# Kernel tuning notes

Hardware: AMD Instinct MI355X
Metric: run time of the kernel (lower is better)

## Reference

```python
import jax, jax.numpy as jnp
import numpy as np

B, N, D = 2, 4096, 256
H = 8
HD = D // H  # head dim = 32
DFF = 4 * D


def _layer_norm(x):
    # Matches source: (x - mean) / (std + 1e-6), std is population std (ddof=0)
    m = jnp.mean(x, axis=-1, keepdims=True)
    s = jnp.std(x, axis=-1, keepdims=True)
    return (x - m) / (s + 1e-6)


def setup_inputs() -> dict:
    key = jax.random.key(0)
    ks = jax.random.split(key, 11)
    sd = 1.0 / np.sqrt(D)
    sf = 1.0 / np.sqrt(DFF)
    return {
        "embeddings_in": jax.random.normal(ks[0], (B, N, D), dtype=jnp.float32),
        "Wq": jax.random.normal(ks[1], (D, D), dtype=jnp.float32) * sd,
        "bq": jnp.zeros((D,), dtype=jnp.float32),
        "Wk": jax.random.normal(ks[2], (D, D), dtype=jnp.float32) * sd,
        "bk": jnp.zeros((D,), dtype=jnp.float32),
        "Wv": jax.random.normal(ks[3], (D, D), dtype=jnp.float32) * sd,
        "bv": jnp.zeros((D,), dtype=jnp.float32),
        "Wo": jax.random.normal(ks[4], (D, D), dtype=jnp.float32) * sd,
        "bo": jnp.zeros((D,), dtype=jnp.float32),
        "W1": jax.random.normal(ks[5], (D, DFF), dtype=jnp.float32) * sd,
        "b1": jnp.zeros((DFF,), dtype=jnp.float32),
        "W2": jax.random.normal(ks[6], (DFF, D), dtype=jnp.float32) * sf,
        "b2": jnp.zeros((D,), dtype=jnp.float32),
    }


def reference(embeddings_in, Wq, bq, Wk, bk, Wv, bv, Wo, bo, W1, b1, W2, b2):
    x = embeddings_in
    xn1 = _layer_norm(x)
    # QKV projections, split into heads: [B,N,D] -> [B,H,N,HD]
    def heads(t):
        return jnp.transpose(t.reshape(B, N, H, HD), (0, 2, 1, 3))
    q = heads(xn1 @ Wq + bq)
    k = heads(xn1 @ Wk + bk)
    v = heads(xn1 @ Wv + bv)
    scores = jnp.einsum('bhnd,bhmd->bhnm', q, k) / jnp.sqrt(jnp.float32(HD))
    attn = jax.nn.softmax(scores, axis=-1)
    heads_out = jnp.einsum('bhnm,bhmd->bhnd', attn, v)
    attn_out = jnp.transpose(heads_out, (0, 2, 1, 3)).reshape(B, N, D)
    attn_out = attn_out @ Wo + bo  # dropout is identity in eval
    x_skip = attn_out + x
    xn2 = _layer_norm(x_skip)
    mlp = jax.nn.gelu(xn2 @ W1 + b1) @ W2 + b2
    return mlp + x_skip
```

## Files before the change

kernel.cpp:

```cpp
#include <hip/hip_runtime.h>
#include <hip/hip_bf16.h>

#define Bb 2
#define Nn 4096
#define Dd 256
#define Hh 8
#define HDh 32
#define DFFd 1024
#define MT (Bb*Nn)
#define Tt ((size_t)MT * Dd)
#define SPLIT 4
#define KVB (Nn / SPLIT)
#define NSTP (KVB / 64)

typedef __attribute__((ext_vector_type(8))) short short8;
typedef __attribute__((ext_vector_type(4))) float f32x4;
typedef __attribute__((address_space(1))) const unsigned int gu32;
typedef __attribute__((address_space(3))) unsigned int lu32;

__device__ __forceinline__ void gll16(const ushort* g, ushort* l) {
  __builtin_amdgcn_global_load_lds((gu32*)g, (lu32*)l, 16, 0, 0);
}
__device__ __forceinline__ float bf2f(ushort u){
  union { unsigned int i; float f; } v; v.i = ((unsigned int)u) << 16; return v.f;
}
__device__ __forceinline__ ushort f2bf(float f){
  union { float f; unsigned int i; } v; v.f = f;
  unsigned int r = v.i + 0x7fffu + ((v.i >> 16) & 1u);
  return (ushort)(r >> 16);
}
__device__ __forceinline__ int ars(int r){ return r * 64 + (r >> 3) * 32; }

__global__ __launch_bounds__(256) void prep_kernel(
    const float* __restrict__ Wq, const float* __restrict__ Wk,
    const float* __restrict__ Wv, const float* __restrict__ Wo,
    const float* __restrict__ W1, const float* __restrict__ W2,
    const float* __restrict__ bq, const float* __restrict__ bk,
    const float* __restrict__ bv, ushort* __restrict__ wt,
    float* __restrict__ bqkv)
{
  const int bid = blockIdx.x, t = threadIdx.x;
  if (bid == 192) {
    bqkv[t] = bq[t]; bqkv[256 + t] = bk[t]; bqkv[512 + t] = bv[t];
    return;
  }
  __shared__ __align__(16) ushort T[64][72];
  const float* src; ushort* dst; int Nsrc, Kdst, kt, nt;
  if (bid < 64) {
    const int m = bid >> 4, tile = bid & 15;
    kt = tile >> 2; nt = tile & 3; Nsrc = 256; Kdst = 256;
    src = (m == 0 ? Wq : m == 1 ? Wk : m == 2 ? Wv : Wo);
    dst = (m == 3) ? (wt + 196608) : (wt + m * 65536);
  } else if (bid < 128) {
    const int tile = bid - 64; kt = tile >> 4; nt = tile & 15;
    Nsrc = 1024; Kdst = 256; src = W1; dst = wt + 262144;
  } else {
    const int tile = bid - 128; kt = tile >> 2; nt = tile & 3;
    Nsrc = 256; Kdst = 1024; src = W2; dst = wt + 524288;
  }
  const int k0 = kt * 64, n0 = nt * 64;
  const int cc = t & 15, rr = t >> 4;
  #pragma unroll
  for (int pass = 0; pass < 4; pass++) {
    const int k = rr + pass * 16;
    const float4 v = *(const float4*)(src + (size_t)(k0 + k) * Nsrc + n0 + cc * 4);
    T[cc * 4 + 0][k] = f2bf(v.x); T[cc * 4 + 1][k] = f2bf(v.y);
    T[cc * 4 + 2][k] = f2bf(v.z); T[cc * 4 + 3][k] = f2bf(v.w);
  }
  __syncthreads();
  const int nl = t >> 2, ks = (t & 3) * 16;
  const short8 a = *(const short8*)(&T[nl][ks]);
  const short8 b = *(const short8*)(&T[nl][ks + 8]);
  ushort* drow = dst + (size_t)(n0 + nl) * Kdst + k0 + ks;
  *(short8*)(drow) = a; *(short8*)(drow + 8) = b;
}

__global__ __launch_bounds__(256) void ln_kernel(const float* __restrict__ x,
                                                 ushort* __restrict__ out)
{
  const int wave = threadIdx.x >> 6, lane = threadIdx.x & 63;
  const int row = blockIdx.x * 4 + wave;
  const float4 u = *(const float4*)(x + (size_t)row * Dd + lane * 4);
  float s1 = u.x + u.y + u.z + u.w;
  float s2 = u.x*u.x + u.y*u.y + u.z*u.z + u.w*u.w;
  #pragma unroll
  for (int m = 1; m < 64; m <<= 1) { s1 += __shfl_xor(s1, m, 64); s2 += __shfl_xor(s2, m, 64); }
  const float mean = s1 * (1.0f / Dd);
  float var = s2 * (1.0f / Dd) - mean * mean;
  var = var < 0.f ? 0.f : var;
  const float inv = 1.0f / (sqrtf(var) + 1e-6f);
  ushort4 o;
  o.x = f2bf((u.x - mean) * inv); o.y = f2bf((u.y - mean) * inv);
  o.z = f2bf((u.z - mean) * inv); o.w = f2bf((u.w - mean) * inv);
  *(ushort4*)(out + (size_t)row * Dd + lane * 4) = o;
}

template<int EPI, int BM>
__global__ __launch_bounds__(256) void gemm_epi(
    const ushort* __restrict__ A, const ushort* __restrict__ BT,
    const float* __restrict__ bias, const float* __restrict__ res,
    void* __restrict__ outv, int N, int K)
{
  constexpr int MI = BM / 64;
  constexpr int AI = BM / 32;
  __shared__ __align__(16) ushort AsF[2][BM * 64 + (BM / 8) * 32];
  __shared__ __align__(16) ushort BsF[2][64 * 64 + 8 * 32];
  const int tid = threadIdx.x;
  const int wave = tid >> 6, lane = tid & 63;
  const int quad = lane >> 4, l15 = lane & 15;
  const int n0 = blockIdx.x * 64, m0 = blockIdx.y * BM;
  f32x4 acc[MI][4];
  #pragma unroll
  for (int mt = 0; mt < MI; mt++)
    #pragma unroll
    for (int nt = 0; nt < 4; nt++) acc[mt][nt] = (f32x4){0.f,0.f,0.f,0.f};
  const int srow = lane >> 3, scol = (lane & 7) * 8;
  const ushort* gA[AI];
  #pragma unroll
  for (int ai = 0; ai < AI; ai++)
    gA[ai] = A + (size_t)(m0 + ai * 32 + wave * 8 + srow) * K + scol;
  const ushort* gB[2];
  #pragma unroll
  for (int bi = 0; bi < 2; bi++)
    gB[bi] = BT + (size_t)(n0 + bi * 32 + wave * 8 + srow) * K + scol;
  int aoff[MI], boff[4];
  #pragma unroll
  for (int mt = 0; mt < MI; mt++) aoff[mt] = ars(wave * 16 * MI + mt * 16 + l15);
  #pragma unroll
  for (int nt = 0; nt < 4; nt++) boff[nt] = ars(nt * 16 + l15);
  #pragma unroll
  for (int ai = 0; ai < AI; ai++) gll16(gA[ai], &AsF[0][ars(ai * 32 + wave * 8)]);
  #pragma unroll
  for (int bi = 0; bi < 2; bi++) gll16(gB[bi], &BsF[0][ars(bi * 32 + wave * 8)]);
  __syncthreads();
  const int NC = K >> 6;
  int p = 0;
  for (int c = 0; c < NC; c++) {
    if (c + 1 < NC) {
      #pragma unroll
      for (int ai = 0; ai < AI; ai++)
        gll16(gA[ai] + (c + 1) * 64, &AsF[p ^ 1][ars(ai * 32 + wave * 8)]);
      #pragma unroll
      for (int bi = 0; bi < 2; bi++)
        gll16(gB[bi] + (c + 1) * 64, &BsF[p ^ 1][ars(bi * 32 + wave * 8)]);
    }
    #pragma unroll
    for (int kk = 0; kk < 2; kk++) {
      short8 af[MI];
      #pragma unroll
      for (int mt = 0; mt < MI; mt++)
        af[mt] = *(const short8*)(&AsF[p][aoff[mt] + kk * 32 + quad * 8]);
      #pragma unroll
      for (int nt = 0; nt < 4; nt++) {
        const short8 bf = *(const short8*)(&BsF[p][boff[nt] + kk * 32 + quad * 8]);
        #pragma unroll
        for (int mt = 0; mt < MI; mt++)
          acc[mt][nt] = __builtin_amdgcn_mfma_f32_16x16x32_bf16(af[mt], bf, acc[mt][nt], 0, 0, 0);
      }
    }
    __syncthreads();
    p ^= 1;
  }
  #pragma unroll
  for (int mt = 0; mt < MI; mt++) {
    const int row0 = m0 + wave * (16 * MI) + mt * 16 + quad * 4;
    #pragma unroll
    for (int nt = 0; nt < 4; nt++) {
      const int col = n0 + nt * 16 + l15;
      const float bv = bias[col];
      float c[4];
      #pragma unroll
      for (int i = 0; i < 4; i++) c[i] = acc[mt][nt][i] + bv;
      if (EPI == 0) {
        ushort* qkv = (ushort*)outv;
        const int w = col >> 8, cd = col & 255;
        const int h = cd >> 5, hd = cd & 31;
        const int b = row0 >> 12, n = row0 & (Nn - 1);
        if (w < 2) {
          const float sc2 = (w == 0) ? (1.4426950408889634f * 0.17677669529663687f) : 1.0f;
          ushort* dst = qkv + (size_t)w * Tt + ((size_t)((b * Hh + h) * Nn) + n) * HDh + hd;
          #pragma unroll
          for (int i = 0; i < 4; i++) dst[(size_t)i * HDh] = f2bf(c[i] * sc2);
        } else {
          ushort4 pk;
          pk.x = f2bf(c[0]); pk.y = f2bf(c[1]); pk.z = f2bf(c[2]); pk.w = f2bf(c[3]);
          *(ushort4*)(qkv + 2 * Tt + ((size_t)((b * Hh + h) * HDh + hd)) * Nn + n) = pk;
        }
      } else if (EPI == 1) {
        float* out = (float*)outv;
        #pragma unroll
        for (int i = 0; i < 4; i++) {
          const size_t idx = (size_t)(row0 + i) * N + col;
          out[idx] = c[i] + res[idx];
        }
      } else {
        ushort* out = (ushort*)outv;
        #pragma unroll
        for (int i = 0; i < 4; i++) {
          const float t = tanhf(0.7978845608028654f * (c[i] + 0.044715f * c[i] * c[i] * c[i]));
          out[(size_t)(row0 + i) * N + col] = f2bf(0.5f * c[i] * (1.0f + t));
        }
      }
    }
  }
}

__global__ __launch_bounds__(256, 4) void attn_kernel(
    const ushort* __restrict__ qp, const ushort* __restrict__ kp,
    const ushort* __restrict__ vtg, ushort* __restrict__ op0,
    ushort* __restrict__ op123, float* __restrict__ lp)
{
  __shared__ __align__(16) ushort Ks[2][64][32];
  __shared__ __align__(16) ushort Vt[2][32][72];
  __shared__ __align__(16) ushort Ps[4][64][40];
  const int tid = threadIdx.x;
  const int wave = tid >> 6, lane = tid & 63;
  const int quad = lane >> 4, l15 = lane & 15;
  const int qtb = blockIdx.x, bh = blockIdx.y, sp = blockIdx.z;
  const size_t base = (size_t)bh * Nn * HDh;
  const int q0 = qtb * 256 + wave * 64;
  short8 qf[4];
  #pragma unroll
  for (int qt = 0; qt < 4; qt++)
    qf[qt] = *(const short8*)(qp + base + (size_t)(q0 + qt * 16 + l15) * HDh + quad * 8);
  const int kv0 = sp * KVB;
  const ushort* kg = kp + base + (size_t)(kv0 + wave * 16 + (lane >> 2)) * HDh + (lane & 3) * 8;
  const int vr = tid >> 3, vc = (tid & 7) * 8;
  const ushort* vg = vtg + base + (size_t)vr * Nn + kv0 + vc;
  ushort* psw = &Ps[wave][0][0];
  f32x4 o[2][4], ol[4];
  #pragma unroll
  for (int qt = 0; qt < 4; qt++) {
    o[0][qt] = (f32x4){0,0,0,0}; o[1][qt] = (f32x4){0,0,0,0};
    ol[qt] = (f32x4){0,0,0,0};
  }
  const short one = (short)0x3F80;
  const short8 ones = {one,one,one,one,one,one,one,one};
  const f32x4 zero4 = {0,0,0,0};
  gll16(kg, &Ks[0][wave * 16][0]);
  int4 vreg = *(const int4*)vg;
  *(int4*)(&Vt[0][vr][vc]) = vreg;
  vreg = *(const int4*)(vg + 64);
  __syncthreads();
  #pragma unroll 2
  for (int step = 0; step < NSTP; step++) {
    const int p = step & 1;
    if (step + 1 < NSTP) {
      gll16(kg + (size_t)(step + 1) * 64 * HDh, &Ks[p ^ 1][wave * 16][0]);
      *(int4*)(&Vt[p ^ 1][vr][vc]) = vreg;
    }
    if (step + 2 < NSTP) vreg = *(const int4*)(vg + (size_t)(step + 2) * 64);
    #pragma unroll
    for (int half = 0; half < 2; half++) {
      #pragma unroll
      for (int nt2 = 0; nt2 < 2; nt2++) {
        const int nt = half * 2 + nt2;
        const short8 kf = *(const short8*)(&Ks[p][nt * 16 + l15][quad * 8]);
        #pragma unroll
        for (int qt = 0; qt < 4; qt++) {
          const f32x4 s = __builtin_amdgcn_mfma_f32_16x16x32_bf16(kf, qf[qt], zero4, 0, 0, 0);
          const float p0 = __builtin_amdgcn_exp2f(s[0]);
          const float p1 = __builtin_amdgcn_exp2f(s[1]);
          const float p2 = __builtin_amdgcn_exp2f(s[2]);
          const float p3 = __builtin_amdgcn_exp2f(s[3]);
          uint2 pk;
          pk.x = __builtin_amdgcn_perm(__float_as_uint(p1) + 0x8000u,
                                       __float_as_uint(p0) + 0x8000u, 0x07060302u);
          pk.y = __builtin_amdgcn_perm(__float_as_uint(p3) + 0x8000u,
                                       __float_as_uint(p2) + 0x8000u, 0x07060302u);
          *(uint2*)(psw + (qt * 16 + l15) * 40 + nt2 * 16 + quad * 4) = pk;
        }
      }
      __builtin_amdgcn_wave_barrier();
      const short8 v0 = *(const short8*)(&Vt[p][l15][half * 32 + quad * 8]);
      const short8 v1 = *(const short8*)(&Vt[p][16 + l15][half * 32 + quad * 8]);
      #pragma unroll
      for (int qt = 0; qt < 4; qt++) {
        const short8 pb = *(const short8*)(psw + (qt * 16 + l15) * 40 + quad * 8);
        o[0][qt] = __builtin_amdgcn_mfma_f32_16x16x32_bf16(v0, pb, o[0][qt], 0, 0, 0);
        o[1][qt] = __builtin_amdgcn_mfma_f32_16x16x32_bf16(v1, pb, o[1][qt], 0, 0, 0);
        ol[qt]   = __builtin_amdgcn_mfma_f32_16x16x32_bf16(ones, pb, ol[qt], 0, 0, 0);
      }
      __builtin_amdgcn_wave_barrier();
    }
    __syncthreads();
  }
  lp[(size_t)sp * (16 * Nn) + (size_t)bh * Nn + q0 + lane] = ol[lane >> 4][0];
  ushort* ob = (sp == 0 ? op0 : op123 + (size_t)(sp - 1) * (16 * (size_t)Nn * HDh));
  #pragma unroll
  for (int pass = 0; pass < 2; pass++) {
    #pragma unroll
    for (int qt2 = 0; qt2 < 2; qt2++) {
      const int qt = pass * 2 + qt2;
      #pragma unroll
      for (int dt = 0; dt < 2; dt++) {
        ushort4 pk;
        pk.x = f2bf(o[dt][qt][0]); pk.y = f2bf(o[dt][qt][1]);
        pk.z = f2bf(o[dt][qt][2]); pk.w = f2bf(o[dt][qt][3]);
        *(ushort4*)(psw + (qt2 * 16 + l15) * 40 + dt * 16 + quad * 4) = pk;
      }
    }
    __builtin_amdgcn_wave_barrier();
    #pragma unroll
    for (int j = 0; j < 2; j++) {
      const int row = j * 16 + (lane >> 2);
      const short8 ov = *(const short8*)(psw + row * 40 + (lane & 3) * 8);
      const int q = q0 + pass * 32 + row;
      *(short8*)(ob + ((size_t)bh * Nn + q) * HDh + (lane & 3) * 8) = ov;
    }
    __builtin_amdgcn_wave_barrier();
  }
}

__global__ __launch_bounds__(256) void attn_combine(
    const ushort* __restrict__ op0, const ushort* __restrict__ op123,
    const float* __restrict__ lp, ushort* __restrict__ attn)
{
  const int idx = blockIdx.x * 256 + threadIdx.x;
  const int d8 = idx & 3, n = (idx >> 2) & (Nn - 1), bh = idx >> 14;
  const size_t ln = (size_t)bh * Nn + n;
  float l = 0.f;
  #pragma unroll
  for (int sp = 0; sp < SPLIT; sp++) l += lp[(size_t)sp * (16 * Nn) + ln];
  const float inv = 1.0f / l;
  float acc[8];
  #pragma unroll
  for (int k = 0; k < 8; k++) acc[k] = 0.f;
  const size_t qoff = ln * HDh + d8 * 8;
  #pragma unroll
  for (int sp = 0; sp < SPLIT; sp++) {
    const ushort* src = (sp == 0 ? op0 : op123 + (size_t)(sp - 1) * (16 * (size_t)Nn * HDh)) + qoff;
    const short8 u = *(const short8*)src;
    #pragma unroll
    for (int k = 0; k < 8; k++) acc[k] += bf2f((ushort)u[k]);
  }
  short8 ov;
  #pragma unroll
  for (int k = 0; k < 8; k++) ov[k] = (short)f2bf(acc[k] * inv);
  const int b = bh >> 3, h = bh & 7;
  *(short8*)(attn + ((size_t)(b * Nn + n)) * Dd + h * HDh + d8 * 8) = ov;
}

extern "C" void kernel_launch(void* const* d_in, const int* in_sizes, int n_in,
                              void* d_out, int out_size, void* d_ws, size_t ws_size,
                              hipStream_t stream)
{
  const float* x  = (const float*)d_in[0];
  const float* Wq = (const float*)d_in[1];
  const float* bq = (const float*)d_in[2];
  const float* Wk = (const float*)d_in[3];
  const float* bk = (const float*)d_in[4];
  const float* Wv = (const float*)d_in[5];
  const float* bv = (const float*)d_in[6];
  const float* Wo = (const float*)d_in[7];
  const float* bo = (const float*)d_in[8];
  const float* W1 = (const float*)d_in[9];
  const float* b1 = (const float*)d_in[10];
  const float* W2 = (const float*)d_in[11];
  const float* b2 = (const float*)d_in[12];

  char* ws = (char*)d_ws;
  ushort* wt    = (ushort*)ws;
  ushort* wtqkv = wt;
  ushort* wto   = wt + 196608;
  ushort* wt1   = wt + 262144;
  ushort* wt2   = wt + 524288;
  float*  bqkv  = (float*)(ws + 786432 * 2);
  ushort* s0    = (ushort*)(ws + 786432 * 2 + 4096);
  ushort* s1    = s0 + Tt;
  ushort* s2    = s1 + Tt;
  ushort* s3    = s2 + Tt;
  float*  xsk   = (float*)(s3 + Tt);
  ushort* xn2   = (ushort*)(xsk + Tt);
  ushort* xn1   = s0;
  ushort* hid   = s0;
  ushort* op0   = s0;
  ushort* op123 = (ushort*)xsk;
  float*  lp    = (float*)d_out;
  ushort* attnb = (ushort*)((char*)d_out + (4u << 20));
  float*  outp  = (float*)d_out;

  const dim3 blk(256);
  hipLaunchKernelGGL(prep_kernel, dim3(193), blk, 0, stream,
                     Wq, Wk, Wv, Wo, W1, W2, bq, bk, bv, wt, bqkv);
  hipLaunchKernelGGL(ln_kernel, dim3(MT / 4), blk, 0, stream, x, xn1);
  hipLaunchKernelGGL((gemm_epi<0,128>), dim3(12, 64), blk, 0, stream,
                     xn1, wtqkv, bqkv, (const float*)nullptr, (void*)s1, 768, Dd);

  hipLaunchKernelGGL(attn_kernel, dim3(Nn / 256, Bb * Hh, SPLIT), blk, 0, stream,
                     s1, s2, s3, op0, op123, lp);
  hipLaunchKernelGGL(attn_combine, dim3((Bb * Hh * Nn * 4) / 256), blk, 0, stream,
                     op0, op123, lp, attnb);

  hipLaunchKernelGGL((gemm_epi<1,64>), dim3(4, 128), blk, 0, stream,
                     attnb, wto, bo, x, (void*)xsk, Dd, Dd);
  hipLaunchKernelGGL(ln_kernel, dim3(MT / 4), blk, 0, stream, xsk, xn2);
  hipLaunchKernelGGL((gemm_epi<2,128>), dim3(16, 64), blk, 0, stream,
                     xn2, wt1, b1, (const float*)nullptr, (void*)hid, DFFd, Dd);
  hipLaunchKernelGGL((gemm_epi<1,64>), dim3(4, 128), blk, 0, stream,
                     hid, wt2, b2, xsk, (void*)outp, Dd, DFFd);
}
```

Measured before the change: 201.6 us.

## Fuse weight prep with first layernorm and drop bf16 rounding in attention

Merges the weight-transpose prep kernel and the first layernorm into a single 512-block launch, removing one kernel launch. Both layernorm kernels now process 16 rows per block instead of 4. The attention P-matrix packing switches from round-to-nearest to truncation when converting to bf16, saving two adds per pair at a small accuracy cost.

```diff
diff --git a/kernel.cpp b/kernel.cpp
--- a/kernel.cpp
+++ b/kernel.cpp
@@ -31,68 +31,79 @@
 }
 __device__ __forceinline__ int ars(int r){ return r * 64 + (r >> 3) * 32; }
 
-__global__ __launch_bounds__(256) void prep_kernel(
+__device__ __forceinline__ void ln_rows4(const float* __restrict__ x,
+                                         ushort* __restrict__ out, int row0,
+                                         int wave, int lane)
+{
+  #pragma unroll
+  for (int r = 0; r < 4; r++) {
+    const int row = row0 + wave * 4 + r;
+    const float4 u = *(const float4*)(x + (size_t)row * Dd + lane * 4);
+    float s1 = u.x + u.y + u.z + u.w;
+    float s2 = u.x*u.x + u.y*u.y + u.z*u.z + u.w*u.w;
+    #pragma unroll
+    for (int m = 1; m < 64; m <<= 1) { s1 += __shfl_xor(s1, m, 64); s2 += __shfl_xor(s2, m, 64); }
+    const float mean = s1 * (1.0f / Dd);
+    float var = s2 * (1.0f / Dd) - mean * mean;
+    var = var < 0.f ? 0.f : var;
+    const float inv = 1.0f / (sqrtf(var) + 1e-6f);
+    ushort4 o;
+    o.x = f2bf((u.x - mean) * inv); o.y = f2bf((u.y - mean) * inv);
+    o.z = f2bf((u.z - mean) * inv); o.w = f2bf((u.w - mean) * inv);
+    *(ushort4*)(out + (size_t)row * Dd + lane * 4) = o;
+  }
+}
+
+__global__ __launch_bounds__(256) void p0_kernel(
     const float* __restrict__ Wq, const float* __restrict__ Wk,
     const float* __restrict__ Wv, const float* __restrict__ Wo,
     const float* __restrict__ W1, const float* __restrict__ W2,
     const float* __restrict__ bq, const float* __restrict__ bk,
     const float* __restrict__ bv, ushort* __restrict__ wt,
-    float* __restrict__ bqkv)
+    float* __restrict__ bqkv, const float* __restrict__ x,
+    ushort* __restrict__ xn1)
 {
   const int bid = blockIdx.x, t = threadIdx.x;
-  if (bid == 192) {
+  __shared__ __align__(16) ushort T[64][72];
+  if (bid < 192) {
+    const float* src; ushort* dst; int Nsrc, Kdst, kt, nt;
+    if (bid < 64) {
+      const int m = bid >> 4, tile = bid & 15;
+      kt = tile >> 2; nt = tile & 3; Nsrc = 256; Kdst = 256;
+      src = (m == 0 ? Wq : m == 1 ? Wk : m == 2 ? Wv : Wo);
+      dst = (m == 3) ? (wt + 196608) : (wt + m * 65536);
+    } else if (bid < 128) {
+      const int tile = bid - 64; kt = tile >> 4; nt = tile & 15;
+      Nsrc = 1024; Kdst = 256; src = W1; dst = wt + 262144;
+    } else {
+      const int tile = bid - 128; kt = tile >> 2; nt = tile & 3;
+      Nsrc = 256; Kdst = 1024; src = W2; dst = wt + 524288;
+    }
+    const int k0 = kt * 64, n0 = nt * 64;
+    const int cc = t & 15, rr = t >> 4;
+    #pragma unroll
+    for (int pass = 0; pass < 4; pass++) {
+      const int k = rr + pass * 16;
+      const float4 v = *(const float4*)(src + (size_t)(k0 + k) * Nsrc + n0 + cc * 4);
+      T[cc * 4 + 0][k] = f2bf(v.x); T[cc * 4 + 1][k] = f2bf(v.y);
+      T[cc * 4 + 2][k] = f2bf(v.z); T[cc * 4 + 3][k] = f2bf(v.w);
+    }
+    __syncthreads();
+    const int nl = t >> 2, ks = (t & 3) * 16;
+    const short8 a = *(const short8*)(&T[nl][ks]);
+    const short8 b = *(const short8*)(&T[nl][ks + 8]);
+    ushort* drow = dst + (size_t)(n0 + nl) * Kdst + k0 + ks;
+    *(short8*)(drow) = a; *(short8*)(drow + 8) = b;
+  } else if (bid == 192) {
     bqkv[t] = bq[t]; bqkv[256 + t] = bk[t]; bqkv[512 + t] = bv[t];
-    return;
-  }
-  __shared__ __align__(16) ushort T[64][72];
-  const float* src; ushort* dst; int Nsrc, Kdst, kt, nt;
-  if (bid < 64) {
-    const int m = bid >> 4, tile = bid & 15;
-    kt = tile >> 2; nt = tile & 3; Nsrc = 256; Kdst = 256;
-    src = (m == 0 ? Wq : m == 1 ? Wk : m == 2 ? Wv : Wo);
-    dst = (m == 3) ? (wt + 196608) : (wt + m * 65536);
-  } else if (bid < 128) {
-    const int tile = bid - 64; kt = tile >> 4; nt = tile & 15;
-    Nsrc = 1024; Kdst = 256; src = W1; dst = wt + 262144;
-  } else {
-    const int tile = bid - 128; kt = tile >> 2; nt = tile & 3;
-    Nsrc = 256; Kdst = 1024; src = W2; dst = wt + 524288;
-  }
-  const int k0 = kt * 64, n0 = nt * 64;
-  const int cc = t & 15, rr = t >> 4;
-  #pragma unroll
-  for (int pass = 0; pass < 4; pass++) {
-    const int k = rr + pass * 16;
-    const float4 v = *(const float4*)(src + (size_t)(k0 + k) * Nsrc + n0 + cc * 4);
-    T[cc * 4 + 0][k] = f2bf(v.x); T[cc * 4 + 1][k] = f2bf(v.y);
-    T[cc * 4 + 2][k] = f2bf(v.z); T[cc * 4 + 3][k] = f2bf(v.w);
-  }
-  __syncthreads();
-  const int nl = t >> 2, ks = (t & 3) * 16;
-  const short8 a = *(const short8*)(&T[nl][ks]);
-  const short8 b = *(const short8*)(&T[nl][ks + 8]);
-  ushort* drow = dst + (size_t)(n0 + nl) * Kdst + k0 + ks;
-  *(short8*)(drow) = a; *(short8*)(drow + 8) = b;
+  }
+  ln_rows4(x, xn1, bid * 16, t >> 6, t & 63);
 }
 
 __global__ __launch_bounds__(256) void ln_kernel(const float* __restrict__ x,
                                                  ushort* __restrict__ out)
 {
-  const int wave = threadIdx.x >> 6, lane = threadIdx.x & 63;
-  const int row = blockIdx.x * 4 + wave;
-  const float4 u = *(const float4*)(x + (size_t)row * Dd + lane * 4);
-  float s1 = u.x + u.y + u.z + u.w;
-  float s2 = u.x*u.x + u.y*u.y + u.z*u.z + u.w*u.w;
-  #pragma unroll
-  for (int m = 1; m < 64; m <<= 1) { s1 += __shfl_xor(s1, m, 64); s2 += __shfl_xor(s2, m, 64); }
-  const float mean = s1 * (1.0f / Dd);
-  float var = s2 * (1.0f / Dd) - mean * mean;
-  var = var < 0.f ? 0.f : var;
-  const float inv = 1.0f / (sqrtf(var) + 1e-6f);
-  ushort4 o;
-  o.x = f2bf((u.x - mean) * inv); o.y = f2bf((u.y - mean) * inv);
-  o.z = f2bf((u.z - mean) * inv); o.w = f2bf((u.w - mean) * inv);
-  *(ushort4*)(out + (size_t)row * Dd + lane * 4) = o;
+  ln_rows4(x, out, blockIdx.x * 16, threadIdx.x >> 6, threadIdx.x & 63);
 }
 
 template<int EPI, int BM>
@@ -264,10 +275,10 @@
           const float p2 = __builtin_amdgcn_exp2f(s[2]);
           const float p3 = __builtin_amdgcn_exp2f(s[3]);
           uint2 pk;
-          pk.x = __builtin_amdgcn_perm(__float_as_uint(p1) + 0x8000u,
-                                       __float_as_uint(p0) + 0x8000u, 0x07060302u);
-          pk.y = __builtin_amdgcn_perm(__float_as_uint(p3) + 0x8000u,
-                                       __float_as_uint(p2) + 0x8000u, 0x07060302u);
+          pk.x = __builtin_amdgcn_perm(__float_as_uint(p1),
+                                       __float_as_uint(p0), 0x07060302u);
+          pk.y = __builtin_amdgcn_perm(__float_as_uint(p3),
+                                       __float_as_uint(p2), 0x07060302u);
           *(uint2*)(psw + (qt * 16 + l15) * 40 + nt2 * 16 + quad * 4) = pk;
         }
       }
@@ -381,9 +392,8 @@
   float*  outp  = (float*)d_out;
 
   const dim3 blk(256);
-  hipLaunchKernelGGL(prep_kernel, dim3(193), blk, 0, stream,
-                     Wq, Wk, Wv, Wo, W1, W2, bq, bk, bv, wt, bqkv);
-  hipLaunchKernelGGL(ln_kernel, dim3(MT / 4), blk, 0, stream, x, xn1);
+  hipLaunchKernelGGL(p0_kernel, dim3(512), blk, 0, stream,
+                     Wq, Wk, Wv, Wo, W1, W2, bq, bk, bv, wt, bqkv, x, xn1);
   hipLaunchKernelGGL((gemm_epi<0,128>), dim3(12, 64), blk, 0, stream,
                      xn1, wtqkv, bqkv, (const float*)nullptr, (void*)s1, 768, Dd);
 
@@ -394,7 +404,7 @@
 
   hipLaunchKernelGGL((gemm_epi<1,64>), dim3(4, 128), blk, 0, stream,
                      attnb, wto, bo, x, (void*)xsk, Dd, Dd);
-  hipLaunchKernelGGL(ln_kernel, dim3(MT / 4), blk, 0, stream, xsk, xn2);
+  hipLaunchKernelGGL(ln_kernel, dim3(MT / 16), blk, 0, stream, xsk, xn2);
   hipLaunchKernelGGL((gemm_epi<2,128>), dim3(16, 64), blk, 0, stream,
                      xn2, wt1, b1, (const float*)nullptr, (void*)hid, DFFd, Dd);
   hipLaunchKernelGGL((gemm_epi<1,64>), dim3(4, 128), blk, 0, stream,
```

After: 197.8 us. About the same (-1.9%).
